# Optimization experiments

Measured on AMD Instinct MI355X. Metric: run time of the kernel, lower is better.

## Reference

```python
import jax, jax.numpy as jnp
import numpy as np

D_MODEL = 1024
N_HEADS = 16
D_K = D_MODEL // N_HEADS
B, S = 2, 2048


def setup_inputs() -> dict:
    key = jax.random.key(0)
    ks = jax.random.split(key, 8)
    scale = 1.0 / np.sqrt(D_MODEL)
    inp = {
        'query': jax.random.normal(ks[0], (B, S, D_MODEL), dtype=jnp.float32),
        'key':   jax.random.normal(ks[1], (B, S, D_MODEL), dtype=jnp.float32),
        'value': jax.random.normal(ks[2], (B, S, D_MODEL), dtype=jnp.float32),
        # causal mask: True = masked (matches masked_fill(mask == True, -1e9))
        'mask': jnp.triu(jnp.ones((1, 1, S, S), dtype=bool), k=1),
        'w_q': jax.random.normal(ks[3], (D_MODEL, D_MODEL), dtype=jnp.float32) * scale,
        'w_k': jax.random.normal(ks[4], (D_MODEL, D_MODEL), dtype=jnp.float32) * scale,
        'w_v': jax.random.normal(ks[5], (D_MODEL, D_MODEL), dtype=jnp.float32) * scale,
        'w_o': jax.random.normal(ks[6], (D_MODEL, D_MODEL), dtype=jnp.float32) * scale,
    }
    return inp


def reference(query, key, value, mask, w_q, w_k, w_v, w_o):
    # nn.Linear stores weight [out, in]; y = x @ W^T
    def split_heads(x, w):
        y = jnp.einsum('bsd,ed->bse', x, w)           # [B,S,D]
        return y.reshape(x.shape[0], x.shape[1], N_HEADS, D_K).transpose(0, 2, 1, 3)  # [B,H,S,dk]

    Q = split_heads(query, w_q)
    K = split_heads(key, w_k)
    V = split_heads(value, w_v)
    scores = jnp.einsum('bhqd,bhkd->bhqk', Q, K) / jnp.sqrt(jnp.float32(D_K))
    scores = jnp.where(mask, jnp.float32(-1e9), scores)
    attn = jax.nn.softmax(scores, axis=-1)            # dropout is identity in eval
    out = jnp.einsum('bhqk,bhkd->bhqd', attn, V)
    out = out.transpose(0, 2, 1, 3).reshape(query.shape[0], query.shape[1], D_MODEL)
    return jnp.einsum('bsd,ed->bse', out, w_o)
```

## Files before the change

### kernel.cpp

```cpp
#include <hip/hip_runtime.h>

#define D_MODEL 1024
#define NH 16
#define DK 64
#define BB 2
#define SS 2048
#define WELEMS (D_MODEL * D_MODEL)
#define XELEMS (BB * SS * D_MODEL)

typedef __attribute__((ext_vector_type(8))) short bf16x8;
typedef __attribute__((ext_vector_type(4))) float f32x4;
typedef __attribute__((ext_vector_type(4))) short s16x4;

__device__ __forceinline__ short f2bf(float f) {
    union { float f; unsigned u; } v; v.f = f;
    unsigned r = v.u + 0x7fffu + ((v.u >> 16) & 1u);
    return (short)(r >> 16);
}

__device__ __forceinline__ float fexp2(float x) {
    float r;
    asm("v_exp_f32 %0, %1" : "=v"(r) : "v"(x));
    return r;
}

__device__ __forceinline__ unsigned pkbf2(float hi, float lo) {
    union { float f; unsigned u; } a, b; a.f = hi; b.f = lo;
    return __builtin_amdgcn_perm(a.u + 0x8000u, b.u + 0x8000u, 0x07060302u);
}

#define AS1 __attribute__((address_space(1)))
#define AS3 __attribute__((address_space(3)))
__device__ __forceinline__ void glds16(const void* g, void* l) {
    __builtin_amdgcn_global_load_lds((AS1 const void*)g, (AS3 void*)l, 16, 0, 0);
}

__global__ __launch_bounds__(256) void convert_all(
    const float* __restrict__ wq, const float* __restrict__ wk,
    const float* __restrict__ wv, const float* __restrict__ wo,
    const float* __restrict__ qi, const float* __restrict__ ki,
    const float* __restrict__ vi, short* __restrict__ dst)
{
    size_t i = ((size_t)blockIdx.x * 256 + threadIdx.x) * 8;
    const float* src;
    size_t off;
    float sc = 1.0f;
    if (i < (size_t)4 * WELEMS) {
        int m = (int)(i >> 20);
        off = i & (WELEMS - 1);
        src = (m == 0) ? wq : (m == 1) ? wk : (m == 2) ? wv : wo;
        if (m == 0) sc = 0.125f * 1.44269504088896340736f;
    } else {
        size_t j = i - (size_t)4 * WELEMS;
        int a = (int)(j >> 22);
        off = j & (XELEMS - 1);
        src = (a == 0) ? qi : (a == 1) ? ki : vi;
    }
    float4 a = *(const float4*)(src + off);
    float4 b = *(const float4*)(src + off + 4);
    bf16x8 pk;
    pk[0] = f2bf(a.x * sc); pk[1] = f2bf(a.y * sc);
    pk[2] = f2bf(a.z * sc); pk[3] = f2bf(a.w * sc);
    pk[4] = f2bf(b.x * sc); pk[5] = f2bf(b.y * sc);
    pk[6] = f2bf(b.z * sc); pk[7] = f2bf(b.w * sc);
    *(bf16x8*)(dst + i) = pk;
}

__global__ __launch_bounds__(256) void qkv_gemm(
    const short* __restrict__ Xall, const short* __restrict__ Wall,
    short* __restrict__ Qo, short* __restrict__ Ko, short* __restrict__ Vo)
{
    const int z = blockIdx.z;
    const short* __restrict__ X = Xall + (size_t)z * XELEMS;
    const short* __restrict__ W = Wall + (size_t)z * WELEMS;

    __shared__ short As[128 * 64];
    __shared__ short Bs[128 * 64];

    const int tid = threadIdx.x;
    const int w = tid >> 6, lane = tid & 63;
    const int l15 = lane & 15, quad = lane >> 4;
    const int wrow = (w >> 1) * 64, wcol = (w & 1) * 64;
    const int m0 = blockIdx.x * 128, n0 = blockIdx.y * 128;
    const int br = lane >> 3, bc = lane & 7;

    f32x4 acc[4][4];
    #pragma unroll
    for (int i = 0; i < 4; ++i)
        #pragma unroll
        for (int j = 0; j < 4; ++j) acc[i][j] = (f32x4){0.f, 0.f, 0.f, 0.f};

    for (int k0 = 0; k0 < D_MODEL; k0 += 64) {
        __syncthreads();
        #pragma unroll
        for (int i = 0; i < 4; ++i) {
            int r = (w * 4 + i) * 8 + br;
            int g = bc ^ (r & 7);
            glds16(X + (size_t)(m0 + r) * D_MODEL + k0 + g * 8, &As[(w * 4 + i) * 512]);
            glds16(W + (size_t)(n0 + r) * D_MODEL + k0 + g * 8, &Bs[(w * 4 + i) * 512]);
        }
        __syncthreads();

        #pragma unroll
        for (int kk = 0; kk < 2; ++kk) {
            const int swz = l15 & 7;
            bf16x8 af[4], bfr[4];
            #pragma unroll
            for (int i = 0; i < 4; ++i) {
                int row = wrow + i * 16 + l15;
                af[i] = *(const bf16x8*)&As[row * 64 + (((kk * 4 + quad) ^ swz) * 8)];
            }
            #pragma unroll
            for (int j = 0; j < 4; ++j) {
                int col = wcol + j * 16 + l15;
                bfr[j] = *(const bf16x8*)&Bs[col * 64 + (((kk * 4 + quad) ^ swz) * 8)];
            }
            #pragma unroll
            for (int i = 0; i < 4; ++i)
                #pragma unroll
                for (int j = 0; j < 4; ++j)
                    acc[i][j] = __builtin_amdgcn_mfma_f32_16x16x32_bf16(af[i], bfr[j], acc[i][j], 0, 0, 0);
        }
    }

    if (z < 2) {
        short* O = z ? Ko : Qo;
        #pragma unroll
        for (int i = 0; i < 4; ++i) {
            int m = m0 + wrow + i * 16 + quad * 4;
            #pragma unroll
            for (int j = 0; j < 4; ++j) {
                int n = n0 + wcol + j * 16 + l15;
                #pragma unroll
                for (int r = 0; r < 4; ++r)
                    O[(size_t)(m + r) * D_MODEL + n] = f2bf(acc[i][j][r]);
            }
        }
    } else {
        const int mbase = m0 + wrow;
        const int b = mbase >> 11, sbase = mbase & (SS - 1);
        #pragma unroll
        for (int j = 0; j < 4; ++j) {
            int n = n0 + wcol + j * 16 + l15;
            int h = n >> 6, d = n & 63;
            short* vdst = Vo + (((size_t)(b * NH + h)) * DK + d) * SS + sbase + quad * 16;
            #pragma unroll
            for (int r = 0; r < 4; ++r) {
                uint2 pk;
                pk.x = pkbf2(acc[1][j][r], acc[0][j][r]);
                pk.y = pkbf2(acc[3][j][r], acc[2][j][r]);
                *(uint2*)(vdst + r * 4) = pk;
            }
        }
    }
}

__global__ __launch_bounds__(512) void attn(
    const short* __restrict__ Q, const short* __restrict__ K,
    const short* __restrict__ V, short* __restrict__ O)
{
    const int x = blockIdx.x;
    const int h = blockIdx.y, b = blockIdx.z;
    const int tid = threadIdx.x, w = tid >> 6, lane = tid & 63;
    const int l15 = lane & 15, quad = lane >> 4;
    const int grp = w >> 2;
    const int wg = w & 3;
    const int qt = grp ? (31 - x) : x;
    const int ktmax = 31 - x;

    __shared__ short Ks[2][64 * 64];
    __shared__ short Vs[2][64 * 64];
    __shared__ short Ps[8][16 * 64];

    const size_t qk_base = ((size_t)b * SS) * D_MODEL + h * DK;
    const short* Kh = K + qk_base;
    const short* Vh = V + ((size_t)(b * NH + h)) * DK * SS;

    const int grow = lane >> 3;
    const int gchunk = (lane & 7) ^ (grow & 7);
    const short* stK = Kh + (size_t)(wg * 16 + grow) * D_MODEL + gchunk * 8;
    const short* stV = Vh + (size_t)(wg * 16 + grow) * SS + gchunk * 8;

    short* const pw = &Ps[w][0];
    const int pswz = l15 & 7;

    bf16x8 qf0, qf1;
    {
        const short* qp = Q + qk_base + (size_t)(qt * 64 + wg * 16 + l15) * D_MODEL;
        qf0 = *(const bf16x8*)(qp + quad * 8);
        qf1 = *(const bf16x8*)(qp + 32 + quad * 8);
    }

    f32x4 oacc[4];
    #pragma unroll
    for (int c = 0; c < 4; ++c) oacc[c] = (f32x4){0.f, 0.f, 0.f, 0.f};
    float lsum[4] = {0.f, 0.f, 0.f, 0.f};

    if (grp == 0) {
        #pragma unroll
        for (int i = 0; i < 2; ++i)
            glds16(stK + (size_t)i * 8 * D_MODEL, &Ks[0][(wg * 16 + i * 8) * 64]);
    } else {
        #pragma unroll
        for (int i = 0; i < 2; ++i)
            glds16(stV + (size_t)i * 8 * SS, &Vs[0][(wg * 16 + i * 8) * 64]);
    }

    int buf = 0;
    for (int kt = 0; kt <= ktmax; ++kt) {
        __syncthreads();
        if (kt < ktmax) {
            const int nb = buf ^ 1;
            if (grp == 0) {
                #pragma unroll
                for (int i = 0; i < 2; ++i)
                    glds16(stK + (size_t)((kt + 1) * 64 + i * 8) * D_MODEL,
                           &Ks[nb][(wg * 16 + i * 8) * 64]);
            } else {
                #pragma unroll
                for (int i = 0; i < 2; ++i)
                    glds16(stV + (size_t)(i * 8) * SS + (kt + 1) * 64,
                           &Vs[nb][(wg * 16 + i * 8) * 64]);
            }
        }

        if (kt <= qt) {
            const short* ksb = &Ks[buf][0];
            const short* vsb = &Vs[buf][0];

            f32x4 sacc[4];
            #pragma unroll
            for (int c = 0; c < 4; ++c) sacc[c] = (f32x4){0.f, 0.f, 0.f, 0.f};
            #pragma unroll
            for (int c = 0; c < 4; ++c) {
                int krow = c * 16 + l15, ksw = krow & 7;
                bf16x8 b0 = *(const bf16x8*)&ksb[krow * 64 + ((quad ^ ksw) * 8)];
                bf16x8 b1 = *(const bf16x8*)&ksb[krow * 64 + (((4 + quad) ^ ksw) * 8)];
                sacc[c] = __builtin_amdgcn_mfma_f32_16x16x32_bf16(qf0, b0, sacc[c], 0, 0, 0);
                sacc[c] = __builtin_amdgcn_mfma_f32_16x16x32_bf16(qf1, b1, sacc[c], 0, 0, 0);
            }

            float pv_[4][4];
            if (kt == qt) {
                const int gq = wg * 16 + quad * 4;
                #pragma unroll
                for (int c = 0; c < 4; ++c) {
                    int ck = c * 16 + l15;
                    #pragma unroll
                    for (int r = 0; r < 4; ++r)
                        pv_[c][r] = (ck <= gq + r) ? fexp2(sacc[c][r]) : 0.f;
                }
            } else {
                #pragma unroll
                for (int c = 0; c < 4; ++c)
                    #pragma unroll
                    for (int r = 0; r < 4; ++r)
                        pv_[c][r] = fexp2(sacc[c][r]);
            }
            #pragma unroll
            for (int r = 0; r < 4; ++r)
                lsum[r] += (pv_[0][r] + pv_[1][r]) + (pv_[2][r] + pv_[3][r]);

            #pragma unroll
            for (int r = 0; r < 4; ++r) {
                int prow = quad * 4 + r;
                int pchunk = (l15 >> 1) ^ (prow & 7);
                uint2 pk;
                pk.x = pkbf2(pv_[1][r], pv_[0][r]);
                pk.y = pkbf2(pv_[3][r], pv_[2][r]);
                *(uint2*)&pw[prow * 64 + pchunk * 8 + (l15 & 1) * 4] = pk;
            }

            #pragma unroll
            for (int kk = 0; kk < 2; ++kk) {
                int u = kk * 4 + quad;
                bf16x8 pf = *(const bf16x8*)&pw[l15 * 64 + ((u ^ pswz) * 8)];
                #pragma unroll
                for (int c = 0; c < 4; ++c) {
                    int vrow = c * 16 + l15;
                    bf16x8 vf = *(const bf16x8*)&vsb[vrow * 64 + ((u ^ (vrow & 7)) * 8)];
                    oacc[c] = __builtin_amdgcn_mfma_f32_16x16x32_bf16(pf, vf, oacc[c], 0, 0, 0);
                }
            }
        }
        buf ^= 1;
    }

    #pragma unroll
    for (int r = 0; r < 4; ++r) {
        float s = lsum[r];
        s += __shfl_xor(s, 1, 64); s += __shfl_xor(s, 2, 64);
        s += __shfl_xor(s, 4, 64); s += __shfl_xor(s, 8, 64);
        lsum[r] = 1.f / s;
    }
    const size_t obase = ((size_t)b * SS + qt * 64 + wg * 16 + quad * 4) * D_MODEL + h * DK;
    #pragma unroll
    for (int r = 0; r < 4; ++r)
        #pragma unroll
        for (int c = 0; c < 4; ++c)
            O[obase + (size_t)r * D_MODEL + c * 16 + l15] = f2bf(oacc[c][r] * lsum[r]);
}

__global__ __launch_bounds__(256) void out_gemm(
    const short* __restrict__ A, const short* __restrict__ W,
    float* __restrict__ C)
{
    __shared__ short As[128 * 64];
    __shared__ short Bs[64 * 64];

    const int tid = threadIdx.x;
    const int w = tid >> 6, lane = tid & 63;
    const int l15 = lane & 15, quad = lane >> 4;
    const int wrow = w * 32;
    const int m0 = blockIdx.x * 128, n0 = blockIdx.y * 64;
    const int br = lane >> 3, bc = lane & 7;

    f32x4 acc[2][4];
    #pragma unroll
    for (int i = 0; i < 2; ++i)
        #pragma unroll
        for (int j = 0; j < 4; ++j) acc[i][j] = (f32x4){0.f, 0.f, 0.f, 0.f};

    for (int k0 = 0; k0 < D_MODEL; k0 += 64) {
        __syncthreads();
        #pragma unroll
        for (int i = 0; i < 4; ++i) {
            int r = (w * 4 + i) * 8 + br;
            int g = bc ^ (r & 7);
            glds16(A + (size_t)(m0 + r) * D_MODEL + k0 + g * 8, &As[(w * 4 + i) * 512]);
        }
        #pragma unroll
        for (int i = 0; i < 2; ++i) {
            int r = (w * 2 + i) * 8 + br;
            int g = bc ^ (r & 7);
            glds16(W + (size_t)(n0 + r) * D_MODEL + k0 + g * 8, &Bs[(w * 2 + i) * 512]);
        }
        __syncthreads();

        #pragma unroll
        for (int kk = 0; kk < 2; ++kk) {
            const int swz = l15 & 7;
            bf16x8 af[2], bfr[4];
            #pragma unroll
            for (int i = 0; i < 2; ++i) {
                int row = wrow + i * 16 + l15;
                af[i] = *(const bf16x8*)&As[row * 64 + (((kk * 4 + quad) ^ swz) * 8)];
            }
            #pragma unroll
            for (int j = 0; j < 4; ++j) {
                int col = j * 16 + l15;
                bfr[j] = *(const bf16x8*)&Bs[col * 64 + (((kk * 4 + quad) ^ swz) * 8)];
            }
            #pragma unroll
            for (int i = 0; i < 2; ++i)
                #pragma unroll
                for (int j = 0; j < 4; ++j)
                    acc[i][j] = __builtin_amdgcn_mfma_f32_16x16x32_bf16(af[i], bfr[j], acc[i][j], 0, 0, 0);
        }
    }

    #pragma unroll
    for (int i = 0; i < 2; ++i) {
        int m = m0 + wrow + i * 16 + quad * 4;
        #pragma unroll
        for (int j = 0; j < 4; ++j) {
            int n = n0 + j * 16 + l15;
            #pragma unroll
            for (int r = 0; r < 4; ++r)
                C[(size_t)(m + r) * D_MODEL + n] = acc[i][j][r];
        }
    }
}

extern "C" void kernel_launch(void* const* d_in, const int* in_sizes, int n_in,
                              void* d_out, int out_size, void* d_ws, size_t ws_size,
                              hipStream_t stream) {
    const float* q  = (const float*)d_in[0];
    const float* k  = (const float*)d_in[1];
    const float* v  = (const float*)d_in[2];
    const float* wq = (const float*)d_in[4];
    const float* wk = (const float*)d_in[5];
    const float* wv = (const float*)d_in[6];
    const float* wo = (const float*)d_in[7];

    short* wbf = (short*)d_ws;
    short* xbf = wbf + 4 * (size_t)WELEMS;
    short* Qb  = xbf + 3 * (size_t)XELEMS;
    short* Kb  = Qb + (size_t)XELEMS;
    short* Vb  = Kb + (size_t)XELEMS;
    short* Ob  = Qb;

    const int conv_elems = 4 * WELEMS + 3 * XELEMS;
    convert_all<<<dim3(conv_elems / (256 * 8)), 256, 0, stream>>>(
        wq, wk, wv, wo, q, k, v, wbf);
    qkv_gemm<<<dim3(32, 8, 3), 256, 0, stream>>>(xbf, wbf, Qb, Kb, Vb);
    attn<<<dim3(16, NH, BB), 512, 0, stream>>>(Qb, Kb, Vb, Ob);
    out_gemm<<<dim3(32, 16), 256, 0, stream>>>(Ob, wbf + 3 * (size_t)WELEMS, (float*)d_out);
}
```

Before: 195.8 us.

## Keep attention probabilities in registers via transposed QK MFMA and permlane swaps

The QK^T MFMA operands are swapped so each lane holds scores for one query row. The exponentiated probabilities are packed to bf16 with v_cvt_pk_bf16_f32 and rearranged into the PV operand layout with permlane32/16 swaps, which removes the per-wave LDS round trip for P and its shared buffer. Row sums now need only a short cross-quad shuffle. The V-projection store is also rewritten to use the hardware pack conversion, and the attention kernel gets a min-blocks launch bound of 4, which may add register pressure.

```diff
diff --git a/kernel.cpp b/kernel.cpp
--- a/kernel.cpp
+++ b/kernel.cpp
@@ -10,7 +10,6 @@
 
 typedef __attribute__((ext_vector_type(8))) short bf16x8;
 typedef __attribute__((ext_vector_type(4))) float f32x4;
-typedef __attribute__((ext_vector_type(4))) short s16x4;
 
 __device__ __forceinline__ short f2bf(float f) {
     union { float f; unsigned u; } v; v.f = f;
@@ -24,9 +23,10 @@
     return r;
 }
 
-__device__ __forceinline__ unsigned pkbf2(float hi, float lo) {
-    union { float f; unsigned u; } a, b; a.f = hi; b.f = lo;
-    return __builtin_amdgcn_perm(a.u + 0x8000u, b.u + 0x8000u, 0x07060302u);
+__device__ __forceinline__ unsigned pkcvt(float lo, float hi) {
+    unsigned r;
+    asm("v_cvt_pk_bf16_f32 %0, %1, %2" : "=v"(r) : "v"(lo), "v"(hi));
+    return r;
 }
 
 #define AS1 __attribute__((address_space(1)))
@@ -143,19 +143,19 @@
         for (int j = 0; j < 4; ++j) {
             int n = n0 + wcol + j * 16 + l15;
             int h = n >> 6, d = n & 63;
-            short* vdst = Vo + (((size_t)(b * NH + h)) * DK + d) * SS + sbase + quad * 16;
-            #pragma unroll
-            for (int r = 0; r < 4; ++r) {
+            short* vdst = Vo + (((size_t)(b * NH + h)) * DK + d) * SS + sbase + quad * 4;
+            #pragma unroll
+            for (int i = 0; i < 4; ++i) {
                 uint2 pk;
-                pk.x = pkbf2(acc[1][j][r], acc[0][j][r]);
-                pk.y = pkbf2(acc[3][j][r], acc[2][j][r]);
-                *(uint2*)(vdst + r * 4) = pk;
-            }
-        }
-    }
-}
-
-__global__ __launch_bounds__(512) void attn(
+                pk.x = pkcvt(acc[i][j][0], acc[i][j][1]);
+                pk.y = pkcvt(acc[i][j][2], acc[i][j][3]);
+                *(uint2*)(vdst + i * 16) = pk;
+            }
+        }
+    }
+}
+
+__global__ __launch_bounds__(512, 4) void attn(
     const short* __restrict__ Q, const short* __restrict__ K,
     const short* __restrict__ V, short* __restrict__ O)
 {
@@ -170,7 +170,6 @@
 
     __shared__ short Ks[2][64 * 64];
     __shared__ short Vs[2][64 * 64];
-    __shared__ short Ps[8][16 * 64];
 
     const size_t qk_base = ((size_t)b * SS) * D_MODEL + h * DK;
     const short* Kh = K + qk_base;
@@ -180,9 +179,6 @@
     const int gchunk = (lane & 7) ^ (grow & 7);
     const short* stK = Kh + (size_t)(wg * 16 + grow) * D_MODEL + gchunk * 8;
     const short* stV = Vh + (size_t)(wg * 16 + grow) * SS + gchunk * 8;
-
-    short* const pw = &Ps[w][0];
-    const int pswz = l15 & 7;
 
     bf16x8 qf0, qf1;
     {
@@ -194,7 +190,7 @@
     f32x4 oacc[4];
     #pragma unroll
     for (int c = 0; c < 4; ++c) oacc[c] = (f32x4){0.f, 0.f, 0.f, 0.f};
-    float lsum[4] = {0.f, 0.f, 0.f, 0.f};
+    float lsum = 0.f;
 
     if (grp == 0) {
         #pragma unroll
@@ -236,49 +232,54 @@
                 int krow = c * 16 + l15, ksw = krow & 7;
                 bf16x8 b0 = *(const bf16x8*)&ksb[krow * 64 + ((quad ^ ksw) * 8)];
                 bf16x8 b1 = *(const bf16x8*)&ksb[krow * 64 + (((4 + quad) ^ ksw) * 8)];
-                sacc[c] = __builtin_amdgcn_mfma_f32_16x16x32_bf16(qf0, b0, sacc[c], 0, 0, 0);
-                sacc[c] = __builtin_amdgcn_mfma_f32_16x16x32_bf16(qf1, b1, sacc[c], 0, 0, 0);
-            }
-
-            float pv_[4][4];
+                sacc[c] = __builtin_amdgcn_mfma_f32_16x16x32_bf16(b0, qf0, sacc[c], 0, 0, 0);
+                sacc[c] = __builtin_amdgcn_mfma_f32_16x16x32_bf16(b1, qf1, sacc[c], 0, 0, 0);
+            }
+
+            float ts = 0.f;
+            unsigned wv[4][2];
             if (kt == qt) {
-                const int gq = wg * 16 + quad * 4;
+                const int qloc = wg * 16 + l15;
                 #pragma unroll
                 for (int c = 0; c < 4; ++c) {
-                    int ck = c * 16 + l15;
+                    float p[4];
                     #pragma unroll
-                    for (int r = 0; r < 4; ++r)
-                        pv_[c][r] = (ck <= gq + r) ? fexp2(sacc[c][r]) : 0.f;
+                    for (int r = 0; r < 4; ++r) {
+                        int kl = c * 16 + quad * 4 + r;
+                        p[r] = (kl <= qloc) ? fexp2(sacc[c][r]) : 0.f;
+                    }
+                    ts += (p[0] + p[1]) + (p[2] + p[3]);
+                    wv[c][0] = pkcvt(p[0], p[1]);
+                    wv[c][1] = pkcvt(p[2], p[3]);
                 }
             } else {
                 #pragma unroll
-                for (int c = 0; c < 4; ++c)
+                for (int c = 0; c < 4; ++c) {
+                    float p[4];
                     #pragma unroll
-                    for (int r = 0; r < 4; ++r)
-                        pv_[c][r] = fexp2(sacc[c][r]);
-            }
-            #pragma unroll
-            for (int r = 0; r < 4; ++r)
-                lsum[r] += (pv_[0][r] + pv_[1][r]) + (pv_[2][r] + pv_[3][r]);
-
-            #pragma unroll
-            for (int r = 0; r < 4; ++r) {
-                int prow = quad * 4 + r;
-                int pchunk = (l15 >> 1) ^ (prow & 7);
-                uint2 pk;
-                pk.x = pkbf2(pv_[1][r], pv_[0][r]);
-                pk.y = pkbf2(pv_[3][r], pv_[2][r]);
-                *(uint2*)&pw[prow * 64 + pchunk * 8 + (l15 & 1) * 4] = pk;
-            }
+                    for (int r = 0; r < 4; ++r) p[r] = fexp2(sacc[c][r]);
+                    ts += (p[0] + p[1]) + (p[2] + p[3]);
+                    wv[c][0] = pkcvt(p[0], p[1]);
+                    wv[c][1] = pkcvt(p[2], p[3]);
+                }
+            }
+            lsum += ts;
 
             #pragma unroll
             for (int kk = 0; kk < 2; ++kk) {
-                int u = kk * 4 + quad;
-                bf16x8 pf = *(const bf16x8*)&pw[l15 * 64 + ((u ^ pswz) * 8)];
+                unsigned j0 = wv[2 * kk][0], j2 = wv[2 * kk + 1][0];
+                unsigned j1 = wv[2 * kk][1], j3 = wv[2 * kk + 1][1];
+                asm("v_permlane32_swap_b32 %0, %1" : "+v"(j0), "+v"(j2));
+                asm("v_permlane16_swap_b32 %0, %1" : "+v"(j0), "+v"(j2));
+                asm("v_permlane32_swap_b32 %0, %1" : "+v"(j1), "+v"(j3));
+                asm("v_permlane16_swap_b32 %0, %1" : "+v"(j1), "+v"(j3));
+                union { unsigned u[4]; bf16x8 v; } pk_;
+                pk_.u[0] = j0; pk_.u[1] = j1; pk_.u[2] = j2; pk_.u[3] = j3;
+                bf16x8 pf = pk_.v;
                 #pragma unroll
                 for (int c = 0; c < 4; ++c) {
                     int vrow = c * 16 + l15;
-                    bf16x8 vf = *(const bf16x8*)&vsb[vrow * 64 + ((u ^ (vrow & 7)) * 8)];
+                    bf16x8 vf = *(const bf16x8*)&vsb[vrow * 64 + (((kk * 4 + quad) ^ (vrow & 7)) * 8)];
                     oacc[c] = __builtin_amdgcn_mfma_f32_16x16x32_bf16(pf, vf, oacc[c], 0, 0, 0);
                 }
             }
@@ -286,19 +287,21 @@
         buf ^= 1;
     }
 
-    #pragma unroll
-    for (int r = 0; r < 4; ++r) {
-        float s = lsum[r];
-        s += __shfl_xor(s, 1, 64); s += __shfl_xor(s, 2, 64);
-        s += __shfl_xor(s, 4, 64); s += __shfl_xor(s, 8, 64);
-        lsum[r] = 1.f / s;
-    }
-    const size_t obase = ((size_t)b * SS + qt * 64 + wg * 16 + quad * 4) * D_MODEL + h * DK;
-    #pragma unroll
-    for (int r = 0; r < 4; ++r)
-        #pragma unroll
-        for (int c = 0; c < 4; ++c)
-            O[obase + (size_t)r * D_MODEL + c * 16 + l15] = f2bf(oacc[c][r] * lsum[r]);
+    {
+        float s = lsum;
+        s += __shfl_xor(s, 16, 64);
+        s += __shfl_xor(s, 32, 64);
+        float inv = 1.f / s;
+        float rinv[4];
+        #pragma unroll
+        for (int r = 0; r < 4; ++r) rinv[r] = __shfl(inv, quad * 4 + r, 16);
+        const size_t obase = ((size_t)b * SS + qt * 64 + wg * 16 + quad * 4) * D_MODEL + h * DK;
+        #pragma unroll
+        for (int r = 0; r < 4; ++r)
+            #pragma unroll
+            for (int c = 0; c < 4; ++c)
+                O[obase + (size_t)r * D_MODEL + c * 16 + l15] = f2bf(oacc[c][r] * rinv[r]);
+    }
 }
 
 __global__ __launch_bounds__(256) void out_gemm(
```

New measurement: 196.2 us. About the same (+0.2%).
